# Performance work log

Measured on AMD Instinct MI355X. Metric: run time of the kernel, lower is better.

The kernel has to match this reference:

```python
import jax, jax.numpy as jnp
import numpy as np

H = 16  # num_heads
T, B, E = 1024, 4, 1024


def _gauss(mu, rho, eps):
    # Bayesian weight sample: sigma = log1p(exp(rho)) = softplus(rho)
    return mu + jax.nn.softplus(rho) * eps


def _rel_shift(x):
    # Transformer-XL relative shift. x: [B, H, Q, K]
    b, h, q, k = x.shape
    x = jnp.pad(x, ((0, 0), (0, 0), (0, 0), (1, 0)))  # zero col at front of K
    x = x.reshape(b, h, k + 1, q)
    return x[:, :, 1:, :].reshape(b, h, q, k)


def setup_inputs() -> dict:
    key = jax.random.key(0)
    ks = iter(jax.random.split(key, 32))
    std = float(np.sqrt(2.0 / (E + E)))

    def nrm(shape, s=std):
        return jax.random.normal(next(ks), shape, dtype=jnp.float32) * s

    def rho(shape):
        return jax.random.uniform(next(ks), shape, dtype=jnp.float32, minval=-5.0, maxval=-4.0)

    inp = {
        'x': jax.random.normal(next(ks), (T, B, E), dtype=jnp.float32),
        'pos': jax.random.normal(next(ks), (T, 1, E), dtype=jnp.float32),
        'attn_mask': jnp.triu(jnp.ones((T, T), dtype=bool), k=1),  # True = masked future
        'in_w_mu': nrm((3 * E, E)), 'in_w_rho': rho((3 * E, E)), 'in_w_eps': nrm((3 * E, E), 1.0),
        'in_b_mu': jnp.zeros((3 * E,), jnp.float32), 'in_b_rho': rho((3 * E,)), 'in_b_eps': nrm((3 * E,), 1.0),
        'pos_w_mu': nrm((E, E)), 'pos_w_rho': rho((E, E)), 'pos_w_eps': nrm((E, E), 1.0),
        'pos_b_mu': jnp.zeros((E,), jnp.float32), 'pos_b_rho': rho((E,)), 'pos_b_eps': nrm((E,), 1.0),
        'out_w_mu': nrm((E, E)), 'out_w_rho': rho((E, E)), 'out_w_eps': nrm((E, E), 1.0),
        'out_b_mu': jnp.zeros((E,), jnp.float32), 'out_b_rho': rho((E,)), 'out_b_eps': nrm((E,), 1.0),
        'rw_mu': nrm((H, E // H)), 'rw_rho': rho((H, E // H)), 'rw_eps': nrm((H, E // H), 1.0),
        'rr_mu': nrm((H, E // H)), 'rr_rho': rho((H, E // H)), 'rr_eps': nrm((H, E // H), 1.0),
    }
    return inp


def reference(x, pos, attn_mask,
              in_w_mu, in_w_rho, in_w_eps, in_b_mu, in_b_rho, in_b_eps,
              pos_w_mu, pos_w_rho, pos_w_eps, pos_b_mu, pos_b_rho, pos_b_eps,
              out_w_mu, out_w_rho, out_w_eps, out_b_mu, out_b_rho, out_b_eps,
              rw_mu, rw_rho, rw_eps, rr_mu, rr_rho, rr_eps):
    t, b, e = x.shape
    d = e // H

    in_w = _gauss(in_w_mu, in_w_rho, in_w_eps)
    in_b = _gauss(in_b_mu, in_b_rho, in_b_eps)
    pos_w = _gauss(pos_w_mu, pos_w_rho, pos_w_eps)
    pos_b = _gauss(pos_b_mu, pos_b_rho, pos_b_eps)
    out_w = _gauss(out_w_mu, out_w_rho, out_w_eps)
    out_b = _gauss(out_b_mu, out_b_rho, out_b_eps)
    r_w_bias = _gauss(rw_mu, rw_rho, rw_eps)  # [H, d]
    r_r_bias = _gauss(rr_mu, rr_rho, rr_eps)  # [H, d]

    qkv = x @ in_w.T + in_b                       # [T, B, 3E]
    q, k, v = jnp.split(qkv, 3, axis=-1)
    q = q.reshape(t, b, H, d)
    k = k.reshape(t, b, H, d)
    v = v.reshape(t, b, H, d)

    r = (pos[:, 0, :] @ pos_w.T + pos_b).reshape(-1, H, d)  # [R, H, d], R == klen

    scale = 1.0 / jnp.sqrt(jnp.asarray(d, x.dtype))
    AC = jnp.einsum('ibhd,jbhd->bhij', q + r_w_bias, k)            # content score
    BD = _rel_shift(jnp.einsum('ibhd,jhd->bhij', q + r_r_bias, r))  # position score
    scores = (AC + BD) * scale                                      # [B, H, T, T]

    neg = jnp.asarray(-1e9, scores.dtype)
    scores = jnp.where(attn_mask[None, None], neg, scores)

    probs = jax.nn.softmax(scores, axis=-1)
    ctx = jnp.einsum('bhij,jbhd->ibhd', probs, v).reshape(t, b, e)
    out = ctx @ out_w.T + out_b                   # [T, B, E]
    return out
```

## Files before the change

### kernel.cpp

```cpp
#include <hip/hip_runtime.h>

typedef unsigned short ushort_t;
typedef __attribute__((ext_vector_type(8))) short short8;
typedef __attribute__((ext_vector_type(4))) float f32x4;
typedef __attribute__((ext_vector_type(4))) unsigned short ush4;

#define MFMA_BF16(a, b, c) __builtin_amdgcn_mfma_f32_16x16x32_bf16((a), (b), (c), 0, 0, 0)

#define GLOAD_LDS16(GP, LP)                                                       \
  __builtin_amdgcn_global_load_lds(                                               \
      (const __attribute__((address_space(1))) void*)(GP),                        \
      (__attribute__((address_space(3))) void*)(LP), 16, 0, 0)

#define T_LEN 1024
#define BATCH 4
#define NHEAD 16
#define DHEAD 64
#define EMB 1024

__device__ __forceinline__ ushort_t f2bf(float f) {
  unsigned u = __float_as_uint(f);
  u += 0x7fffu + ((u >> 16) & 1u);
  return (ushort_t)(u >> 16);
}

__global__ void sample_w_kernel(const float* __restrict__ im, const float* __restrict__ ir,
                                const float* __restrict__ ie, ushort_t* __restrict__ io,
                                const float* __restrict__ pm, const float* __restrict__ pr,
                                const float* __restrict__ pe, ushort_t* __restrict__ po,
                                const float* __restrict__ om, const float* __restrict__ orh,
                                const float* __restrict__ oe, ushort_t* __restrict__ oo) {
  int i = blockIdx.x * 256 + threadIdx.x;
  const float *mu, *rho, *eps;
  ushort_t* out;
  int j;
  if (i < 786432) { mu = im; rho = ir; eps = ie; out = io; j = i; }
  else if (i < 1048576) { mu = pm; rho = pr; eps = pe; out = po; j = i - 786432; }
  else { mu = om; rho = orh; eps = oe; out = oo; j = i - 1048576; }
  f32x4 m = *(const f32x4*)(mu + (size_t)j * 4);
  f32x4 r = *(const f32x4*)(rho + (size_t)j * 4);
  f32x4 e = *(const f32x4*)(eps + (size_t)j * 4);
  ush4 o;
#pragma unroll
  for (int k = 0; k < 4; ++k) o[k] = f2bf(m[k] + log1pf(__expf(r[k])) * e[k]);
  *(ush4*)(out + (size_t)j * 4) = o;
}

__global__ void sample_bias_kernel(
    const float* __restrict__ am, const float* __restrict__ ar, const float* __restrict__ ae, float* __restrict__ ao,
    const float* __restrict__ bm, const float* __restrict__ br, const float* __restrict__ be, float* __restrict__ bo,
    const float* __restrict__ cm, const float* __restrict__ cr, const float* __restrict__ ce, float* __restrict__ co,
    const float* __restrict__ dm, const float* __restrict__ dr, const float* __restrict__ de, float* __restrict__ dof,
    const float* __restrict__ em, const float* __restrict__ er, const float* __restrict__ ee, float* __restrict__ eo) {
  int i = blockIdx.x * 256 + threadIdx.x;
  if (i < 3072) {
    ao[i] = am[i] + log1pf(__expf(ar[i])) * ae[i];
  } else if (i < 4096) {
    int j = i - 3072; bo[j] = bm[j] + log1pf(__expf(br[j])) * be[j];
  } else if (i < 5120) {
    int j = i - 4096; co[j] = cm[j] + log1pf(__expf(cr[j])) * ce[j];
  } else if (i < 6144) {
    int j = i - 5120; dof[j] = dm[j] + log1pf(__expf(dr[j])) * de[j];
  } else if (i < 7168) {
    int j = i - 6144; eo[j] = em[j] + log1pf(__expf(er[j])) * ee[j];
  }
}

__global__ void cast_bf16x4_kernel(const float* __restrict__ in, ushort_t* __restrict__ out, int n4) {
  int i = blockIdx.x * 256 + threadIdx.x;
  if (i < n4) {
    f32x4 v = *(const f32x4*)(in + (size_t)i * 4);
    ush4 o;
#pragma unroll
    for (int j = 0; j < 4; ++j) o[j] = f2bf(v[j]);
    *(ush4*)(out + (size_t)i * 4) = o;
  }
}

__global__ void zero_rhp_pad_kernel(ushort_t* __restrict__ rhp) {
  int idx = blockIdx.x * 256 + threadIdx.x;
  int dd = idx & 63;
  int pr = (idx >> 6) & 127;
  int h = idx >> 13;
  int phys = (pr < 64) ? pr : (pr - 64 + 1088);
  rhp[((size_t)h * 1152 + phys) * 64 + dd] = 0;
}

__global__ __launch_bounds__(256, 2)
void gemm_bt_kernel(const ushort_t* __restrict__ A, const ushort_t* __restrict__ Bt,
                    const float* __restrict__ bias, float* __restrict__ C,
                    int M, int N, int K) {
  __shared__ ushort_t As[128 * 32];
  __shared__ ushort_t Bs[128 * 32];
  const int tid = threadIdx.x;
  const int w = tid >> 6, l = tid & 63;
  const int m0 = blockIdx.x * 128, n0 = blockIdx.y * 128;
  const int wr = w >> 1, wc = w & 1;
  const int fr = l & 15, fk = (l >> 4) * 8;

  f32x4 acc[4][4] = {};

  for (int k0 = 0; k0 < K; k0 += 32) {
    __syncthreads();
#pragma unroll
    for (int p = 0; p < 2; ++p) {
      int c = p * 256 + tid;
      int row = c >> 2, col = (c & 3) * 8;
      GLOAD_LDS16(&A[(size_t)(m0 + row) * K + k0 + col], &As[c * 8]);
      GLOAD_LDS16(&Bt[(size_t)(n0 + row) * K + k0 + col], &Bs[c * 8]);
    }
    __syncthreads();
    short8 af[4], bf[4];
#pragma unroll
    for (int mi = 0; mi < 4; ++mi) af[mi] = *(const short8*)(&As[(wr * 64 + mi * 16 + fr) * 32 + fk]);
#pragma unroll
    for (int ni = 0; ni < 4; ++ni) bf[ni] = *(const short8*)(&Bs[(wc * 64 + ni * 16 + fr) * 32 + fk]);
#pragma unroll
    for (int mi = 0; mi < 4; ++mi)
#pragma unroll
      for (int ni = 0; ni < 4; ++ni)
        acc[mi][ni] = MFMA_BF16(af[mi], bf[ni], acc[mi][ni]);
  }

#pragma unroll
  for (int ni = 0; ni < 4; ++ni) {
    int col = n0 + wc * 64 + ni * 16 + fr;
    float bv = bias[col];
#pragma unroll
    for (int mi = 0; mi < 4; ++mi) {
#pragma unroll
      for (int q = 0; q < 4; ++q) {
        int row = m0 + wr * 64 + mi * 16 + (l >> 4) * 4 + q;
        C[(size_t)row * N + col] = acc[mi][ni][q] + bv;
      }
    }
  }
}

__global__ __launch_bounds__(256, 2)
void gemm_qkvpos_kernel(const ushort_t* __restrict__ x_bf, const ushort_t* __restrict__ in_w_bf,
                        const float* __restrict__ in_b,
                        const float* __restrict__ rwb, const float* __restrict__ rrb,
                        const ushort_t* __restrict__ posx_bf, const ushort_t* __restrict__ pos_w_bf,
                        const float* __restrict__ pos_b,
                        ushort_t* __restrict__ qrw, ushort_t* __restrict__ qrr,
                        ushort_t* __restrict__ kbuf, ushort_t* __restrict__ vt,
                        ushort_t* __restrict__ rhp) {
  __shared__ ushort_t As[128 * 32];
  __shared__ ushort_t Bs[128 * 32];
  const int K = 1024;
  const int tid = threadIdx.x;
  const int w = tid >> 6, l = tid & 63;
  const int bid = blockIdx.x;
  const bool isPos = bid >= 768;
  int m0, n0;
  const ushort_t *A, *Bt;
  if (!isPos) {
    m0 = (bid & 31) * 128; n0 = (bid >> 5) * 128; A = x_bf; Bt = in_w_bf;
  } else {
    int pb2 = bid - 768;
    m0 = (pb2 & 7) * 128; n0 = (pb2 >> 3) * 128; A = posx_bf; Bt = pos_w_bf;
  }
  const int wr = w >> 1, wc = w & 1;
  const int fr = l & 15, fk = (l >> 4) * 8;

  f32x4 acc[4][4] = {};

  for (int k0 = 0; k0 < K; k0 += 32) {
    __syncthreads();
#pragma unroll
    for (int p = 0; p < 2; ++p) {
      int c = p * 256 + tid;
      int row = c >> 2, col = (c & 3) * 8;
      GLOAD_LDS16(&A[(size_t)(m0 + row) * K + k0 + col], &As[c * 8]);
      GLOAD_LDS16(&Bt[(size_t)(n0 + row) * K + k0 + col], &Bs[c * 8]);
    }
    __syncthreads();
    short8 af[4], bf[4];
#pragma unroll
    for (int mi = 0; mi < 4; ++mi) af[mi] = *(const short8*)(&As[(wr * 64 + mi * 16 + fr) * 32 + fk]);
#pragma unroll
    for (int ni = 0; ni < 4; ++ni) bf[ni] = *(const short8*)(&Bs[(wc * 64 + ni * 16 + fr) * 32 + fk]);
#pragma unroll
    for (int mi = 0; mi < 4; ++mi)
#pragma unroll
      for (int ni = 0; ni < 4; ++ni)
        acc[mi][ni] = MFMA_BF16(af[mi], bf[ni], acc[mi][ni]);
  }

  if (!isPos) {
#pragma unroll
    for (int ni = 0; ni < 4; ++ni) {
      int col = n0 + wc * 64 + ni * 16 + fr;
      int part = col >> 10;
      int e = col & 1023;
      int hh = e >> 6, dd = e & 63;
      float bv = in_b[col];
      float rwv = rwb[e];
      float rrv = rrb[e];
#pragma unroll
      for (int mi = 0; mi < 4; ++mi) {
#pragma unroll
        for (int q = 0; q < 4; ++q) {
          int row = m0 + wr * 64 + mi * 16 + (l >> 4) * 4 + q;
          int t = row >> 2, b = row & 3;
          float v = acc[mi][ni][q] + bv;
          if (part == 0) {
            unsigned idx = (((unsigned)(b * 16 + hh) * 1024 + t) << 6) + dd;
            qrw[idx] = f2bf(v + rwv);
            qrr[idx] = f2bf(v + rrv);
          } else if (part == 1) {
            unsigned idx = (((unsigned)(b * 16 + hh) * 1024 + t) << 6) + dd;
            kbuf[idx] = f2bf(v);
          } else {
            vt[(((unsigned)(b * 16 + hh) * 64 + dd) << 10) + t] = f2bf(v);
          }
        }
      }
    }
  } else {
#pragma unroll
    for (int ni = 0; ni < 4; ++ni) {
      int col = n0 + wc * 64 + ni * 16 + fr;
      int hh = col >> 6, dd = col & 63;
      float bv = pos_b[col];
#pragma unroll
      for (int mi = 0; mi < 4; ++mi) {
#pragma unroll
        for (int q = 0; q < 4; ++q) {
          int t = m0 + wr * 64 + mi * 16 + (l >> 4) * 4 + q;
          rhp[((unsigned)hh * 1152 + 64 + t) * 64 + dd] = f2bf(acc[mi][ni][q] + bv);
        }
      }
    }
  }
}

__global__ __launch_bounds__(256, 2)
void attn_kernel(const ushort_t* __restrict__ qrw, const ushort_t* __restrict__ qrr,
                 const ushort_t* __restrict__ kb, const ushort_t* __restrict__ vt,
                 const ushort_t* __restrict__ rhp, ushort_t* __restrict__ ctx) {
  __shared__ __attribute__((aligned(16))) ushort_t KV[2][8192];
  __shared__ __attribute__((aligned(16))) char PtB[4][2048];

  const int tid = threadIdx.x, w = tid >> 6, l = tid & 63;
  const int bid = blockIdx.x;
  const int g = bid & 63;
  const int h = ((g & 7) << 1) | ((g >> 3) & 1);
  const int b = g >> 4;
  const int bh = b * 16 + h;
  const int p = bid >> 6;
  const int istA = (15 - p) * 64 + w * 16;
  const int istB = p * 64 + w * 16;
  const int njt = 16 - p;
  const int njtB = p + 1;
  const int fr = l & 15, fkq = (l >> 4) * 8;
  const float scale = 0.125f;
  char* Pw = PtB[w];

  short8 aqwA0, aqwA1, aqrA0, aqrA1, aqwB0, aqwB1, aqrB0, aqrB1;
  {
    unsigned qa = ((unsigned)bh * T_LEN + istA + fr) * 64 + fkq;
    aqwA0 = *(const short8*)(qrw + qa);
    aqwA1 = *(const short8*)(qrw + qa + 32);
    aqrA0 = *(const short8*)(qrr + qa);
    aqrA1 = *(const short8*)(qrr + qa + 32);
    unsigned qb = ((unsigned)bh * T_LEN + istB + fr) * 64 + fkq;
    aqwB0 = *(const short8*)(qrw + qb);
    aqwB1 = *(const short8*)(qrw + qb + 32);
    aqrB0 = *(const short8*)(qrr + qb);
    aqrB1 = *(const short8*)(qrr + qb + 32);
  }

  const int srow = 16 * w + (l >> 3);
  const unsigned sswz = (unsigned)(((l & 7) ^ (l >> 3)) << 4);
  const unsigned kgcol = (unsigned)(l & 7) * 8;
  const unsigned swzr = (unsigned)(fr & 7) << 4;

  const unsigned rbaseA = ((unsigned)h * 1152 + 64 + 1008 - istA + fr) * 64 + fkq;
  const unsigned rbaseB = ((unsigned)h * 1152 + 64 + 1008 - istB + fr) * 64 + fkq;

  float sA[4] = {0.f, 0.f, 0.f, 0.f}, sB[4] = {0.f, 0.f, 0.f, 0.f};
  f32x4 oA[4] = {}, oB[4] = {};

  short8 sg0, sg1, sg2, sg3;
#define STAGE_LOAD(J0)                                                              \
  do {                                                                              \
    sg0 = *(const short8*)(kb + ((unsigned)bh * 1024 + (unsigned)(J0) + srow) * 64 + kgcol);      \
    sg1 = *(const short8*)(kb + ((unsigned)bh * 1024 + (unsigned)(J0) + srow + 8) * 64 + kgcol);  \
    sg2 = *(const short8*)(vt + ((unsigned)bh * 64 + srow) * 1024 + (unsigned)(J0) + kgcol);      \
    sg3 = *(const short8*)(vt + ((unsigned)bh * 64 + srow + 8) * 1024 + (unsigned)(J0) + kgcol);  \
  } while (0)
#define STAGE_WRITE(BUF)                                                            \
  do {                                                                              \
    char* KS_ = (char*)KV[BUF];                                                     \
    *(short8*)(KS_ + (unsigned)srow * 128 + sswz) = sg0;                            \
    *(short8*)(KS_ + (unsigned)(srow + 8) * 128 + sswz) = sg1;                      \
    *(short8*)(KS_ + 8192 + (unsigned)srow * 128 + sswz) = sg2;                     \
    *(short8*)(KS_ + 8192 + (unsigned)(srow + 8) * 128 + sswz) = sg3;               \
  } while (0)

#define STRIP_TILE(AQW0, AQW1, AQR0, AQR1, RBASE, IST, SRUN, OACC)                   \
  do {                                                                               \
    short8 rf[10];                                                                   \
    unsigned roff = (RBASE) + (unsigned)j0 * 64;                                     \
    _Pragma("unroll")                                                                \
    for (int f = 0; f < 5; ++f) {                                                    \
      rf[2 * f] = *(const short8*)(rhp + roff + f * 1024);                           \
      rf[2 * f + 1] = *(const short8*)(rhp + roff + f * 1024 + 32);                  \
    }                                                                                \
    f32x4 ac[4] = {};                                                                \
    f32x4 pb[5] = {};                                                                \
    {                                                                                \
      short8 kf[8];                                                                  \
      _Pragma("unroll")                                                              \
      for (int f = 0; f < 4; ++f) {                                                  \
        unsigned rowb = (unsigned)(f * 16 + fr) * 128;                               \
        kf[2 * f] = *(const short8*)(KS + rowb + (((unsigned)fkq * 2) ^ swzr));      \
        kf[2 * f + 1] = *(const short8*)(KS + rowb + (((unsigned)fkq * 2 + 64) ^ swzr)); \
      }                                                                              \
      _Pragma("unroll")                                                              \
      for (int f = 0; f < 4; ++f) {                                                  \
        ac[f] = MFMA_BF16(AQW0, kf[2 * f], ac[f]);                                   \
        ac[f] = MFMA_BF16(AQW1, kf[2 * f + 1], ac[f]);                               \
      }                                                                              \
      _Pragma("unroll")                                                              \
      for (int f = 0; f < 5; ++f) {                                                  \
        pb[f] = MFMA_BF16(AQR0, rf[2 * f], pb[f]);                                   \
        pb[f] = MFMA_BF16(AQR1, rf[2 * f + 1], pb[f]);                               \
      }                                                                              \
    }                                                                                \
    _Pragma("unroll")                                                                \
    for (int q = 0; q < 4; ++q) {                                                    \
      int ri = 4 * (l >> 4) + q;                                                     \
      int e = 15 + fr - ri;                                                          \
      int src = (l & 48) | (e & 15);                                                 \
      float sh[5];                                                                   \
      _Pragma("unroll")                                                              \
      for (int f = 0; f < 5; ++f) sh[f] = __shfl(pb[f][q], src, 64);                 \
      int hi = e >> 4;                                                               \
      int ig = (IST) + ri;                                                           \
      _Pragma("unroll")                                                              \
      for (int ni = 0; ni < 4; ++ni) {                                               \
        float pv = hi ? sh[ni + 1] : sh[ni];                                         \
        float s = (ac[ni][q] + pv) * scale - 20.0f;                                  \
        int jg = j0 + ni * 16 + fr;                                                  \
        float pp = (jg > ig) ? 0.f : __expf(s);                                      \
        *(ushort_t*)(Pw + (((ri * 128) + (ni * 16 + fr) * 2) ^ ((ri & 7) << 4))) = f2bf(pp); \
        SRUN[q] += pp;                                                               \
      }                                                                              \
    }                                                                                \
    {                                                                                \
      short8 vf[8];                                                                  \
      _Pragma("unroll")                                                              \
      for (int dg = 0; dg < 4; ++dg) {                                               \
        unsigned rowb = 8192 + (unsigned)(dg * 16 + fr) * 128;                       \
        vf[2 * dg] = *(const short8*)(KS + rowb + (((unsigned)fkq * 2) ^ swzr));     \
        vf[2 * dg + 1] = *(const short8*)(KS + rowb + (((unsigned)(64 + fkq * 2)) ^ swzr)); \
      }                                                                              \
      short8 pa0 = *(const short8*)(Pw + ((fr * 128 + fkq * 2) ^ ((fr & 7) << 4)));  \
      short8 pa1 = *(const short8*)(Pw + ((fr * 128 + 64 + fkq * 2) ^ ((fr & 7) << 4))); \
      _Pragma("unroll")                                                              \
      for (int dg = 0; dg < 4; ++dg) {                                               \
        OACC[dg] = MFMA_BF16(pa0, vf[2 * dg], OACC[dg]);                             \
        OACC[dg] = MFMA_BF16(pa1, vf[2 * dg + 1], OACC[dg]);                         \
      }                                                                              \
    }                                                                                \
  } while (0)

  STAGE_LOAD(0);
  STAGE_WRITE(0);
  __syncthreads();

  for (int jt = 0; jt < njt; ++jt) {
    const int j0 = jt << 6;
    const char* KS = (const char*)KV[jt & 1];

    if (jt + 1 < njt) STAGE_LOAD((jt + 1) << 6);

    STRIP_TILE(aqwA0, aqwA1, aqrA0, aqrA1, rbaseA, istA, sA, oA);
    if (jt < njtB) STRIP_TILE(aqwB0, aqwB1, aqrB0, aqrB1, rbaseB, istB, sB, oB);

    if (jt + 1 < njt) STAGE_WRITE((jt + 1) & 1);
    __syncthreads();
  }

#pragma unroll
  for (int q = 0; q < 4; ++q) {
    float a = sA[q], bq = sB[q];
#pragma unroll
    for (int o2 = 8; o2; o2 >>= 1) {
      a += __shfl_xor(a, o2, 64);
      bq += __shfl_xor(bq, o2, 64);
    }
    sA[q] = a;
    sB[q] = bq;
  }
#pragma unroll
  for (int dg = 0; dg < 4; ++dg) {
#pragma unroll
    for (int q = 0; q < 4; ++q) {
      int dd = dg * 16 + fr;
      int igA = istA + 4 * (l >> 4) + q;
      ctx[((size_t)igA * BATCH + b) * EMB + h * 64 + dd] = f2bf(oA[dg][q] / sA[q]);
      int igB = istB + 4 * (l >> 4) + q;
      ctx[((size_t)igB * BATCH + b) * EMB + h * 64 + dd] = f2bf(oB[dg][q] / sB[q]);
    }
  }
}

extern "C" void kernel_launch(void* const* d_in, const int* in_sizes, int n_in,
                              void* d_out, int out_size, void* d_ws, size_t ws_size,
                              hipStream_t stream) {
  (void)in_sizes; (void)n_in; (void)out_size; (void)ws_size;
  const float* x = (const float*)d_in[0];
  const float* pos = (const float*)d_in[1];
  const float* in_w_mu = (const float*)d_in[3];
  const float* in_w_rho = (const float*)d_in[4];
  const float* in_w_eps = (const float*)d_in[5];
  const float* in_b_mu = (const float*)d_in[6];
  const float* in_b_rho = (const float*)d_in[7];
  const float* in_b_eps = (const float*)d_in[8];
  const float* pos_w_mu = (const float*)d_in[9];
  const float* pos_w_rho = (const float*)d_in[10];
  const float* pos_w_eps = (const float*)d_in[11];
  const float* pos_b_mu = (const float*)d_in[12];
  const float* pos_b_rho = (const float*)d_in[13];
  const float* pos_b_eps = (const float*)d_in[14];
  const float* out_w_mu = (const float*)d_in[15];
  const float* out_w_rho = (const float*)d_in[16];
  const float* out_w_eps = (const float*)d_in[17];
  const float* out_b_mu = (const float*)d_in[18];
  const float* out_b_rho = (const float*)d_in[19];
  const float* out_b_eps = (const float*)d_in[20];
  const float* rw_mu = (const float*)d_in[21];
  const float* rw_rho = (const float*)d_in[22];
  const float* rw_eps = (const float*)d_in[23];
  const float* rr_mu = (const float*)d_in[24];
  const float* rr_rho = (const float*)d_in[25];
  const float* rr_eps = (const float*)d_in[26];

  char* ws = (char*)d_ws;
  ushort_t* in_w_bf  = (ushort_t*)(ws + 0);
  ushort_t* pos_w_bf = (ushort_t*)(ws + 6291456);
  ushort_t* out_w_bf = (ushort_t*)(ws + 8388608);
  float* in_b  = (float*)(ws + 10485760);
  float* pos_b = (float*)(ws + 10498048);
  float* out_b = (float*)(ws + 10502144);
  float* rwb   = (float*)(ws + 10506240);
  float* rrb   = (float*)(ws + 10510336);
  ushort_t* x_bf    = (ushort_t*)(ws + 10514432);
  ushort_t* posx_bf = (ushort_t*)(ws + 18903040);
  ushort_t* qrw = (ushort_t*)(ws + 21000192);
  ushort_t* qrr = (ushort_t*)(ws + 29388800);
  ushort_t* kb  = (ushort_t*)(ws + 37777408);
  ushort_t* vt  = (ushort_t*)(ws + 46166016);
  ushort_t* rhp = (ushort_t*)(ws + 54554624);
  ushort_t* ctx = (ushort_t*)(ws + 56913920);

  sample_w_kernel<<<5120, 256, 0, stream>>>(in_w_mu, in_w_rho, in_w_eps, in_w_bf,
                                            pos_w_mu, pos_w_rho, pos_w_eps, pos_w_bf,
                                            out_w_mu, out_w_rho, out_w_eps, out_w_bf);
  sample_bias_kernel<<<28, 256, 0, stream>>>(in_b_mu, in_b_rho, in_b_eps, in_b,
                                             pos_b_mu, pos_b_rho, pos_b_eps, pos_b,
                                             out_b_mu, out_b_rho, out_b_eps, out_b,
                                             rw_mu, rw_rho, rw_eps, rwb,
                                             rr_mu, rr_rho, rr_eps, rrb);
  cast_bf16x4_kernel<<<4096, 256, 0, stream>>>(x, x_bf, 1048576);
  cast_bf16x4_kernel<<<1024, 256, 0, stream>>>(pos, posx_bf, 262144);
  zero_rhp_pad_kernel<<<512, 256, 0, stream>>>(rhp);

  gemm_qkvpos_kernel<<<832, 256, 0, stream>>>(x_bf, in_w_bf, in_b, rwb, rrb,
                                              posx_bf, pos_w_bf, pos_b,
                                              qrw, qrr, kb, vt, rhp);

  attn_kernel<<<dim3(512), 256, 0, stream>>>(qrw, qrr, kb, vt, rhp, ctx);

  gemm_bt_kernel<<<dim3(32, 8), 256, 0, stream>>>(ctx, out_w_bf, out_b, (float*)d_out, 4096, 1024, 1024);
}
```

Baseline: 202.8 us.

## Split attention into one strip per block with 32-wide K tiles and direct LDS loads

Measured after the change: 169.9 us. 16.2% less time.

```diff
diff --git a/kernel.cpp b/kernel.cpp
--- a/kernel.cpp
+++ b/kernel.cpp
@@ -240,8 +240,8 @@
 void attn_kernel(const ushort_t* __restrict__ qrw, const ushort_t* __restrict__ qrr,
                  const ushort_t* __restrict__ kb, const ushort_t* __restrict__ vt,
                  const ushort_t* __restrict__ rhp, ushort_t* __restrict__ ctx) {
-  __shared__ __attribute__((aligned(16))) ushort_t KV[2][8192];
-  __shared__ __attribute__((aligned(16))) char PtB[4][2048];
+  __shared__ __attribute__((aligned(16))) ushort_t KV[2][4096];
+  __shared__ __attribute__((aligned(16))) char PtB[4][1024];
 
   const int tid = threadIdx.x, w = tid >> 6, l = tid & 63;
   const int bid = blockIdx.x;
@@ -249,162 +249,134 @@
   const int h = ((g & 7) << 1) | ((g >> 3) & 1);
   const int b = g >> 4;
   const int bh = b * 16 + h;
-  const int p = bid >> 6;
-  const int istA = (15 - p) * 64 + w * 16;
-  const int istB = p * 64 + w * 16;
-  const int njt = 16 - p;
-  const int njtB = p + 1;
+  const int sx = 15 - (bid >> 6);
+  const int istrip = sx * 64 + w * 16;
   const int fr = l & 15, fkq = (l >> 4) * 8;
   const float scale = 0.125f;
   char* Pw = PtB[w];
-
-  short8 aqwA0, aqwA1, aqrA0, aqrA1, aqwB0, aqwB1, aqrB0, aqrB1;
+  const int njt = (sx + 1) * 2;
+  const int jlim = istrip + 15;
+  const unsigned swzr = (unsigned)(fr & 7) << 4;
+  const unsigned swzp = (unsigned)((fr >> 1) & 3) << 4;
+
+  short8 aqw0, aqw1, aqr0, aqr1;
   {
-    unsigned qa = ((unsigned)bh * T_LEN + istA + fr) * 64 + fkq;
-    aqwA0 = *(const short8*)(qrw + qa);
-    aqwA1 = *(const short8*)(qrw + qa + 32);
-    aqrA0 = *(const short8*)(qrr + qa);
-    aqrA1 = *(const short8*)(qrr + qa + 32);
-    unsigned qb = ((unsigned)bh * T_LEN + istB + fr) * 64 + fkq;
-    aqwB0 = *(const short8*)(qrw + qb);
-    aqwB1 = *(const short8*)(qrw + qb + 32);
-    aqrB0 = *(const short8*)(qrr + qb);
-    aqrB1 = *(const short8*)(qrr + qb + 32);
-  }
-
-  const int srow = 16 * w + (l >> 3);
-  const unsigned sswz = (unsigned)(((l & 7) ^ (l >> 3)) << 4);
-  const unsigned kgcol = (unsigned)(l & 7) * 8;
-  const unsigned swzr = (unsigned)(fr & 7) << 4;
-
-  const unsigned rbaseA = ((unsigned)h * 1152 + 64 + 1008 - istA + fr) * 64 + fkq;
-  const unsigned rbaseB = ((unsigned)h * 1152 + 64 + 1008 - istB + fr) * 64 + fkq;
-
-  float sA[4] = {0.f, 0.f, 0.f, 0.f}, sB[4] = {0.f, 0.f, 0.f, 0.f};
-  f32x4 oA[4] = {}, oB[4] = {};
-
-  short8 sg0, sg1, sg2, sg3;
-#define STAGE_LOAD(J0)                                                              \
-  do {                                                                              \
-    sg0 = *(const short8*)(kb + ((unsigned)bh * 1024 + (unsigned)(J0) + srow) * 64 + kgcol);      \
-    sg1 = *(const short8*)(kb + ((unsigned)bh * 1024 + (unsigned)(J0) + srow + 8) * 64 + kgcol);  \
-    sg2 = *(const short8*)(vt + ((unsigned)bh * 64 + srow) * 1024 + (unsigned)(J0) + kgcol);      \
-    sg3 = *(const short8*)(vt + ((unsigned)bh * 64 + srow + 8) * 1024 + (unsigned)(J0) + kgcol);  \
+    unsigned qb = ((unsigned)bh * T_LEN + istrip + fr) * 64 + fkq;
+    aqw0 = *(const short8*)(qrw + qb);
+    aqw1 = *(const short8*)(qrw + qb + 32);
+    aqr0 = *(const short8*)(qrr + qb);
+    aqr1 = *(const short8*)(qrr + qb + 32);
+  }
+
+  const int krow = tid >> 3;
+  const int kci8 = ((tid & 7) ^ (krow & 7)) * 8;
+  const int vdr = tid >> 2;
+  const int vci8 = ((tid & 3) ^ ((vdr >> 1) & 3)) * 8;
+  const ushort_t* kgbase = kb + ((unsigned)bh * 1024 + krow) * 64 + kci8;
+  const ushort_t* vgbase = vt + ((unsigned)bh * 64 + vdr) * 1024 + vci8;
+
+  const unsigned rbase = ((unsigned)h * 1152 + 64 + 1008 - istrip + fr) * 64 + fkq;
+
+  float s_run[4] = {0.f, 0.f, 0.f, 0.f};
+  f32x4 o[4] = {};
+
+#define STAGE(J0, BUF)                                                    \
+  do {                                                                    \
+    ushort_t* Kd = (ushort_t*)KV[BUF];                                    \
+    GLOAD_LDS16(kgbase + (unsigned)(J0) * 64, Kd + tid * 8);              \
+    GLOAD_LDS16(vgbase + (unsigned)(J0), Kd + 2048 + tid * 8);            \
   } while (0)
-#define STAGE_WRITE(BUF)                                                            \
-  do {                                                                              \
-    char* KS_ = (char*)KV[BUF];                                                     \
-    *(short8*)(KS_ + (unsigned)srow * 128 + sswz) = sg0;                            \
-    *(short8*)(KS_ + (unsigned)(srow + 8) * 128 + sswz) = sg1;                      \
-    *(short8*)(KS_ + 8192 + (unsigned)srow * 128 + sswz) = sg2;                     \
-    *(short8*)(KS_ + 8192 + (unsigned)(srow + 8) * 128 + sswz) = sg3;               \
-  } while (0)
-
-#define STRIP_TILE(AQW0, AQW1, AQR0, AQR1, RBASE, IST, SRUN, OACC)                   \
-  do {                                                                               \
-    short8 rf[10];                                                                   \
-    unsigned roff = (RBASE) + (unsigned)j0 * 64;                                     \
-    _Pragma("unroll")                                                                \
-    for (int f = 0; f < 5; ++f) {                                                    \
-      rf[2 * f] = *(const short8*)(rhp + roff + f * 1024);                           \
-      rf[2 * f + 1] = *(const short8*)(rhp + roff + f * 1024 + 32);                  \
-    }                                                                                \
-    f32x4 ac[4] = {};                                                                \
-    f32x4 pb[5] = {};                                                                \
-    {                                                                                \
-      short8 kf[8];                                                                  \
-      _Pragma("unroll")                                                              \
-      for (int f = 0; f < 4; ++f) {                                                  \
-        unsigned rowb = (unsigned)(f * 16 + fr) * 128;                               \
-        kf[2 * f] = *(const short8*)(KS + rowb + (((unsigned)fkq * 2) ^ swzr));      \
-        kf[2 * f + 1] = *(const short8*)(KS + rowb + (((unsigned)fkq * 2 + 64) ^ swzr)); \
-      }                                                                              \
-      _Pragma("unroll")                                                              \
-      for (int f = 0; f < 4; ++f) {                                                  \
-        ac[f] = MFMA_BF16(AQW0, kf[2 * f], ac[f]);                                   \
-        ac[f] = MFMA_BF16(AQW1, kf[2 * f + 1], ac[f]);                               \
-      }                                                                              \
-      _Pragma("unroll")                                                              \
-      for (int f = 0; f < 5; ++f) {                                                  \
-        pb[f] = MFMA_BF16(AQR0, rf[2 * f], pb[f]);                                   \
-        pb[f] = MFMA_BF16(AQR1, rf[2 * f + 1], pb[f]);                               \
-      }                                                                              \
-    }                                                                                \
-    _Pragma("unroll")                                                                \
-    for (int q = 0; q < 4; ++q) {                                                    \
-      int ri = 4 * (l >> 4) + q;                                                     \
-      int e = 15 + fr - ri;                                                          \
-      int src = (l & 48) | (e & 15);                                                 \
-      float sh[5];                                                                   \
-      _Pragma("unroll")                                                              \
-      for (int f = 0; f < 5; ++f) sh[f] = __shfl(pb[f][q], src, 64);                 \
-      int hi = e >> 4;                                                               \
-      int ig = (IST) + ri;                                                           \
-      _Pragma("unroll")                                                              \
-      for (int ni = 0; ni < 4; ++ni) {                                               \
-        float pv = hi ? sh[ni + 1] : sh[ni];                                         \
-        float s = (ac[ni][q] + pv) * scale - 20.0f;                                  \
-        int jg = j0 + ni * 16 + fr;                                                  \
-        float pp = (jg > ig) ? 0.f : __expf(s);                                      \
-        *(ushort_t*)(Pw + (((ri * 128) + (ni * 16 + fr) * 2) ^ ((ri & 7) << 4))) = f2bf(pp); \
-        SRUN[q] += pp;                                                               \
-      }                                                                              \
-    }                                                                                \
-    {                                                                                \
-      short8 vf[8];                                                                  \
-      _Pragma("unroll")                                                              \
-      for (int dg = 0; dg < 4; ++dg) {                                               \
-        unsigned rowb = 8192 + (unsigned)(dg * 16 + fr) * 128;                       \
-        vf[2 * dg] = *(const short8*)(KS + rowb + (((unsigned)fkq * 2) ^ swzr));     \
-        vf[2 * dg + 1] = *(const short8*)(KS + rowb + (((unsigned)(64 + fkq * 2)) ^ swzr)); \
-      }                                                                              \
-      short8 pa0 = *(const short8*)(Pw + ((fr * 128 + fkq * 2) ^ ((fr & 7) << 4)));  \
-      short8 pa1 = *(const short8*)(Pw + ((fr * 128 + 64 + fkq * 2) ^ ((fr & 7) << 4))); \
-      _Pragma("unroll")                                                              \
-      for (int dg = 0; dg < 4; ++dg) {                                               \
-        OACC[dg] = MFMA_BF16(pa0, vf[2 * dg], OACC[dg]);                             \
-        OACC[dg] = MFMA_BF16(pa1, vf[2 * dg + 1], OACC[dg]);                         \
-      }                                                                              \
-    }                                                                                \
-  } while (0)
-
-  STAGE_LOAD(0);
-  STAGE_WRITE(0);
+
+  STAGE(0, 0);
   __syncthreads();
 
   for (int jt = 0; jt < njt; ++jt) {
-    const int j0 = jt << 6;
-    const char* KS = (const char*)KV[jt & 1];
-
-    if (jt + 1 < njt) STAGE_LOAD((jt + 1) << 6);
-
-    STRIP_TILE(aqwA0, aqwA1, aqrA0, aqrA1, rbaseA, istA, sA, oA);
-    if (jt < njtB) STRIP_TILE(aqwB0, aqwB1, aqrB0, aqrB1, rbaseB, istB, sB, oB);
-
-    if (jt + 1 < njt) STAGE_WRITE((jt + 1) & 1);
+    const int j0 = jt << 5;
+    const int buf = jt & 1;
+    if (jt + 1 < njt) STAGE((jt + 1) << 5, buf ^ 1);
+
+    if (j0 <= jlim) {
+      const char* KS = (const char*)KV[buf];
+
+      short8 rf[6];
+      {
+        unsigned roff = rbase + (unsigned)j0 * 64;
+#pragma unroll
+        for (int f = 0; f < 3; ++f) {
+          rf[2 * f] = *(const short8*)(rhp + roff + f * 1024);
+          rf[2 * f + 1] = *(const short8*)(rhp + roff + f * 1024 + 32);
+        }
+      }
+      f32x4 ac0 = {0, 0, 0, 0}, ac1 = {0, 0, 0, 0};
+      f32x4 pb0 = {0, 0, 0, 0}, pb1 = {0, 0, 0, 0}, pb2 = {0, 0, 0, 0};
+      {
+        short8 kf00 = *(const short8*)(KS + (unsigned)fr * 128 + (((unsigned)fkq * 2) ^ swzr));
+        short8 kf01 = *(const short8*)(KS + (unsigned)fr * 128 + (((unsigned)(64 + fkq * 2)) ^ swzr));
+        short8 kf10 = *(const short8*)(KS + (unsigned)(16 + fr) * 128 + (((unsigned)fkq * 2) ^ swzr));
+        short8 kf11 = *(const short8*)(KS + (unsigned)(16 + fr) * 128 + (((unsigned)(64 + fkq * 2)) ^ swzr));
+        ac0 = MFMA_BF16(aqw0, kf00, ac0);
+        ac0 = MFMA_BF16(aqw1, kf01, ac0);
+        ac1 = MFMA_BF16(aqw0, kf10, ac1);
+        ac1 = MFMA_BF16(aqw1, kf11, ac1);
+      }
+      pb0 = MFMA_BF16(aqr0, rf[0], pb0);
+      pb0 = MFMA_BF16(aqr1, rf[1], pb0);
+      pb1 = MFMA_BF16(aqr0, rf[2], pb1);
+      pb1 = MFMA_BF16(aqr1, rf[3], pb1);
+      pb2 = MFMA_BF16(aqr0, rf[4], pb2);
+      pb2 = MFMA_BF16(aqr1, rf[5], pb2);
+
+#pragma unroll
+      for (int q = 0; q < 4; ++q) {
+        int ri = 4 * (l >> 4) + q;
+        int e = 15 + fr - ri;
+        int src = (l & 48) | (e & 15);
+        float sh0 = __shfl(pb0[q], src, 64);
+        float sh1 = __shfl(pb1[q], src, 64);
+        float sh2 = __shfl(pb2[q], src, 64);
+        int hi = e >> 4;
+        float pv0 = hi ? sh1 : sh0;
+        float pv1 = hi ? sh2 : sh1;
+        int ig = istrip + ri;
+        float s0 = (ac0[q] + pv0) * scale - 20.0f;
+        float s1 = (ac1[q] + pv1) * scale - 20.0f;
+        float p0 = (j0 + fr > ig) ? 0.f : __expf(s0);
+        float p1 = (j0 + 16 + fr > ig) ? 0.f : __expf(s1);
+        unsigned psw = (unsigned)((ri >> 1) & 3) << 4;
+        *(ushort_t*)(Pw + ri * 64 + (((unsigned)(fr * 2)) ^ psw)) = f2bf(p0);
+        *(ushort_t*)(Pw + ri * 64 + (((unsigned)(32 + fr * 2)) ^ psw)) = f2bf(p1);
+        s_run[q] += p0 + p1;
+      }
+
+      {
+        short8 pa = *(const short8*)(Pw + (unsigned)fr * 64 + (((unsigned)fkq * 2) ^ swzp));
+#pragma unroll
+        for (int dg = 0; dg < 4; ++dg) {
+          int vrow = dg * 16 + fr;
+          short8 vf = *(const short8*)(KS + 4096 + (unsigned)vrow * 64 +
+                                       (((unsigned)fkq * 2) ^ ((unsigned)((vrow >> 1) & 3) << 4)));
+          o[dg] = MFMA_BF16(pa, vf, o[dg]);
+        }
+      }
+    }
+
     __syncthreads();
   }
 
 #pragma unroll
   for (int q = 0; q < 4; ++q) {
-    float a = sA[q], bq = sB[q];
-#pragma unroll
-    for (int o2 = 8; o2; o2 >>= 1) {
-      a += __shfl_xor(a, o2, 64);
-      bq += __shfl_xor(bq, o2, 64);
-    }
-    sA[q] = a;
-    sB[q] = bq;
+    float sq = s_run[q];
+#pragma unroll
+    for (int o2 = 8; o2; o2 >>= 1) sq += __shfl_xor(sq, o2, 64);
+    s_run[q] = sq;
   }
 #pragma unroll
   for (int dg = 0; dg < 4; ++dg) {
 #pragma unroll
     for (int q = 0; q < 4; ++q) {
+      int ig = istrip + 4 * (l >> 4) + q;
       int dd = dg * 16 + fr;
-      int igA = istA + 4 * (l >> 4) + q;
-      ctx[((size_t)igA * BATCH + b) * EMB + h * 64 + dd] = f2bf(oA[dg][q] / sA[q]);
-      int igB = istB + 4 * (l >> 4) + q;
-      ctx[((size_t)igB * BATCH + b) * EMB + h * 64 + dd] = f2bf(oB[dg][q] / sB[q]);
+      ctx[((size_t)ig * BATCH + b) * EMB + h * 64 + dd] = f2bf(o[dg][q] / s_run[q]);
     }
   }
 }
@@ -474,7 +446,7 @@
                                               posx_bf, pos_w_bf, pos_b,
                                               qrw, qrr, kb, vt, rhp);
 
-  attn_kernel<<<dim3(512), 256, 0, stream>>>(qrw, qrr, kb, vt, rhp, ctx);
+  attn_kernel<<<dim3(1024), 256, 0, stream>>>(qrw, qrr, kb, vt, rhp, ctx);
 
   gemm_bt_kernel<<<dim3(32, 8), 256, 0, stream>>>(ctx, out_w_bf, out_b, (float*)d_out, 4096, 1024, 1024);
 }
```
